# Kernel tuning notes

Hardware: AMD Instinct MI355X
Metric: run time of the kernel (lower is better)

## Reference

```python
import jax, jax.numpy as jnp
import numpy as np
from jax.scipy.linalg import solve_triangular

CHUNK = 32


def _l2norm(x):
    return x / jnp.sqrt(jnp.sum(x * x, axis=-1, keepdims=True))


def setup_inputs() -> dict:
    key = jax.random.key(0)
    kq, kk, kv, kb = jax.random.split(key, 4)
    b, h, L, d = 2, 8, 4096, 128
    q = jax.random.normal(kq, (b, h, L, d), dtype=jnp.float32)
    k = jax.random.normal(kk, (b, h, L, d), dtype=jnp.float32)
    v = jax.random.normal(kv, (b, h, L, d), dtype=jnp.float32)
    beta = jax.random.uniform(kb, (b, h, L), dtype=jnp.float32)
    return {"q": q, "k": k, "v": v, "beta": beta}


def _delta_rule_chunkwise(q, k, v, beta, chunk_size=CHUNK):
    b, h, L, d_k = q.shape
    d_v = v.shape[-1]
    pad_len = (-L) % chunk_size
    if pad_len:
        q = jnp.pad(q, ((0, 0), (0, 0), (0, pad_len), (0, 0)))
        k = jnp.pad(k, ((0, 0), (0, 0), (0, pad_len), (0, 0)))
        v = jnp.pad(v, ((0, 0), (0, 0), (0, pad_len), (0, 0)))
        beta = jnp.pad(beta, ((0, 0), (0, 0), (0, pad_len)))
    L_pad = L + pad_len
    n = L_pad // chunk_size
    c = chunk_size

    q = _l2norm(q)
    k = _l2norm(k)
    v = v * beta[..., None]
    k_beta = k * beta[..., None]

    # -> [b, h, n, c, d]
    qc = q.reshape(b, h, n, c, d_k)
    kc = k.reshape(b, h, n, c, d_k)
    vc = v.reshape(b, h, n, c, d_v)
    kbc = k_beta.reshape(b, h, n, c, d_k)

    # Intra-chunk UT transform: inv = (I + strictly_lower(k_beta @ k^T))^{-1}
    # (equivalent to the sequential forward-substitution loop in the torch code)
    A = jnp.einsum('bhnce,bhnfe->bhncf', kbc, kc)          # [b,h,n,c,c]
    strict_lower = jnp.tril(jnp.ones((c, c), dtype=A.dtype), k=-1)
    T = A * strict_lower + jnp.eye(c, dtype=A.dtype)        # unit lower-triangular
    eye_b = jnp.broadcast_to(jnp.eye(c, dtype=A.dtype), T.shape)
    inv = solve_triangular(T, eye_b, lower=True)            # [b,h,n,c,c]

    u = jnp.einsum('bhncf,bhnfd->bhncd', inv, vc)           # [b,h,n,c,d_v]
    w = jnp.einsum('bhncf,bhnfk->bhnck', inv, kbc)          # [b,h,n,c,d_k]

    # Cross-chunk recurrence over n chunks (sequential in n)
    causal = jnp.tril(jnp.ones((c, c), dtype=q.dtype))      # incl. diagonal
    qs = jnp.moveaxis(qc, 2, 0)   # [n,b,h,c,d_k]
    ks = jnp.moveaxis(kc, 2, 0)
    us = jnp.moveaxis(u, 2, 0)
    ws = jnp.moveaxis(w, 2, 0)

    S0 = jnp.zeros((b, h, d_k, d_v), dtype=q.dtype)

    def step(S, xs):
        q_i, k_i, u_i, w_i = xs
        local_attn = jnp.einsum('bhce,bhfe->bhcf', q_i, k_i) * causal
        u_adj = u_i - jnp.einsum('bhck,bhkd->bhcd', w_i, S)
        o_i = jnp.einsum('bhck,bhkd->bhcd', q_i, S) \
            + jnp.einsum('bhcf,bhfd->bhcd', local_attn, u_adj)
        S_new = S + jnp.einsum('bhck,bhcd->bhkd', k_i, u_adj)
        return S_new, o_i

    S_final, outs = jax.lax.scan(step, S0, (qs, ks, us, ws))
    out = jnp.moveaxis(outs, 0, 2).reshape(b, h, L_pad, d_v)
    if pad_len:
        out = out[:, :, :L]
    return out, S_final


def reference(q, k, v, beta):
    return _delta_rule_chunkwise(q, k, v, beta)
```

## Files before the change

### kernel.cpp

```cpp
#include <hip/hip_runtime.h>


#define Bb 2
#define Hh 8
#define Ll 4096
#define Dd 128
#define DP (Dd + 4)
#define Cc 32
#define CP2 33
#define NC (Ll / Cc)
#define BHn (Bb * Hh)

#define SLAB 20480

typedef float  f32x16 __attribute__((ext_vector_type(16)));
typedef short  bf16x8 __attribute__((ext_vector_type(8)));

__device__ __forceinline__ short f2bf(float x) {
    union { float f; unsigned u; } a; a.f = x;
    const unsigned r = a.u + 0x7FFFu + ((a.u >> 16) & 1u);
    return (short)(r >> 16);
}

__device__ __forceinline__ float bf2f(short h) {
    union { unsigned u; float f; } t;
    t.u = ((unsigned)(unsigned short)h) << 16;
    return t.f;
}

__device__ __forceinline__ unsigned cvt_pk_bf16(float lo, float hi) {
    unsigned r;
    asm("v_cvt_pk_bf16_f32 %0, %1, %2" : "=v"(r) : "v"(lo), "v"(hi));
    return r;
}

__device__ __forceinline__ bf16x8 mk_bop(const f32x16& T, int m) {
    const int o = 8 * m;
    const unsigned a01 = cvt_pk_bf16(T[o + 0], T[o + 1]);
    const unsigned a23 = cvt_pk_bf16(T[o + 2], T[o + 3]);
    const unsigned b01 = cvt_pk_bf16(T[o + 4], T[o + 5]);
    const unsigned b23 = cvt_pk_bf16(T[o + 6], T[o + 7]);
    const auto r0 = __builtin_amdgcn_permlane32_swap(a01, b01, false, false);
    const auto r1 = __builtin_amdgcn_permlane32_swap(a23, b23, false, false);
    union { unsigned u[4]; bf16x8 v; } out;
    out.u[0] = r0[0]; out.u[1] = r1[0]; out.u[2] = r0[1]; out.u[3] = r1[1];
    return out.v;
}

__device__ __forceinline__ void gl_lds16(const void* gsrc, void* ldst) {
    __builtin_amdgcn_global_load_lds(
        (const __attribute__((address_space(1))) unsigned int*)gsrc,
        (__attribute__((address_space(3))) unsigned int*)ldst, 16, 0, 0);
}

__device__ __forceinline__ void split8(const float4& a, const float4& b,
                                       bf16x8& hi, bf16x8& lo) {
    const float x[8] = {a.x, a.y, a.z, a.w, b.x, b.y, b.z, b.w};
    #pragma unroll
    for (int j = 0; j < 8; ++j) {
        const short hs = f2bf(x[j]);
        hi[j] = hs;
        lo[j] = f2bf(x[j] - bf2f(hs));
    }
}

__device__ __forceinline__ void fma4(float4& acc, float s, const float4& x) {
    acc.x += s * x.x; acc.y += s * x.y; acc.z += s * x.z; acc.w += s * x.w;
}

template <bool QNB>
__global__ __launch_bounds__(256, 4) void prep_kernel(
    const float* __restrict__ q, const float* __restrict__ k,
    const float* __restrict__ v, const float* __restrict__ beta,
    float* __restrict__ wsU, float* __restrict__ wsNq,
    short* __restrict__ wsWb, short* __restrict__ wsKtb,
    short* __restrict__ wsAttnb, short* __restrict__ wsQnb)
{
    __shared__ float sK[Cc][DP];
    __shared__ float sA[Cc][CP2];
    __shared__ float sInv[Cc][CP2];
    __shared__ float sBeta[Cc], sNk[Cc], sNq[Cc];

    const int tid = threadIdx.x;
    const int blk = blockIdx.x;
    const int bh = blk / NC;
    const int ch = blk % NC;
    const size_t base = (size_t)(bh * Ll + ch * Cc) * Dd;

    for (int e = tid; e < Cc * Dd / 4; e += 256) {
        const int r = e >> 5, c4 = e & 31;
        ((float4*)&sK[r][0])[c4] = ((const float4*)(k + base))[e];
    }
    if (tid < Cc) sBeta[tid] = beta[bh * Ll + ch * Cc + tid];
    __syncthreads();

    {
        const int row = tid >> 2, part = tid & 3;
        float s = 0.f;
        if (row < Cc) {
            const float4* src = (const float4*)&sK[row][0];
            #pragma unroll
            for (int j = 0; j < 8; ++j) {
                const float4 t = src[part + j * 4];
                s += t.x * t.x + t.y * t.y + t.z * t.z + t.w * t.w;
            }
        } else {
            const float4* src =
                (const float4*)(q + base + (size_t)(row - Cc) * Dd);
            #pragma unroll
            for (int j = 0; j < 8; ++j) {
                const float4 t = src[part + j * 4];
                s += t.x * t.x + t.y * t.y + t.z * t.z + t.w * t.w;
            }
        }
        s += __shfl_xor(s, 1);
        s += __shfl_xor(s, 2);
        if (part == 0) {
            const float r = 1.0f / sqrtf(s);
            if (row < Cc) sNk[row] = r; else sNq[row - Cc] = r;
        }
    }
    __syncthreads();

    if (tid < Cc) wsNq[bh * Ll + ch * Cc + tid] = sNq[tid];

    for (int e = tid; e < Cc * Dd / 4; e += 256) {
        const int r = e >> 5, c4 = e & 31;
        float4 kk = ((float4*)&sK[r][0])[c4];
        const float nk = sNk[r];
        kk.x *= nk; kk.y *= nk; kk.z *= nk; kk.w *= nk;
        ((float4*)&sK[r][0])[c4] = kk;
    }
    __syncthreads();

    const int wid = tid >> 6;
    const int lc = tid & 31;
    const int lh = (tid >> 5) & 1;
    const size_t cbase = (size_t)blk * Cc * Dd;
    const size_t abase = (size_t)blk * Cc * Cc;

    if (wid == 0) {
        f32x16 D, D2;
        #pragma unroll
        for (int r = 0; r < 16; ++r) { D[r] = 0.f; D2[r] = 0.f; }
        #pragma unroll
        for (int ks = 0; ks < 8; ++ks) {
            const float4 a = ((const float4*)&sK[lc][0])[4 * ks + 2 * lh];
            const float4 b = ((const float4*)&sK[lc][0])[4 * ks + 2 * lh + 1];
            bf16x8 hi, lo;
            split8(a, b, hi, lo);
            D  = __builtin_amdgcn_mfma_f32_32x32x16_bf16(hi, hi, D,  0, 0, 0);
            D2 = __builtin_amdgcn_mfma_f32_32x32x16_bf16(hi, lo, D2, 0, 0, 0);
            D2 = __builtin_amdgcn_mfma_f32_32x32x16_bf16(lo, hi, D2, 0, 0, 0);
        }
        #pragma unroll
        for (int r = 0; r < 16; ++r) {
            const int row = (r & 3) + 8 * (r >> 2) + 4 * lh;
            sA[row][lc] = (D[r] + D2[r]) * sBeta[row];
        }
        asm volatile("s_waitcnt lgkmcnt(0)" ::: "memory");
        __builtin_amdgcn_sched_barrier(0);

        float inv[Cc];
        #pragma unroll
        for (int m = 0; m < Cc; ++m) inv[m] = (m == lc) ? 1.f : 0.f;
        #pragma unroll
        for (int i = 1; i < Cc; ++i) {
            float s = 0.f;
            #pragma unroll
            for (int m = 0; m < i; ++m) s += sA[i][m] * inv[m];
            inv[i] = (lc == i) ? 1.f : -s;
        }
        if (lh == 0) {
            #pragma unroll
            for (int m = 0; m < Cc; ++m) sInv[m][lc] = inv[m];
        }
    } else if (wid == 1) {
        const float nq = sNq[lc];
        const float* qrow = q + base + (size_t)lc * Dd;
        f32x16 D, D2;
        #pragma unroll
        for (int r = 0; r < 16; ++r) { D[r] = 0.f; D2[r] = 0.f; }
        #pragma unroll
        for (int ks = 0; ks < 8; ++ks) {
            float4 a = ((const float4*)qrow)[4 * ks + 2 * lh];
            float4 b = ((const float4*)qrow)[4 * ks + 2 * lh + 1];
            a.x *= nq; a.y *= nq; a.z *= nq; a.w *= nq;
            b.x *= nq; b.y *= nq; b.z *= nq; b.w *= nq;
            bf16x8 hiQ, loQ;
            split8(a, b, hiQ, loQ);
            const float4 ka = ((const float4*)&sK[lc][0])[4 * ks + 2 * lh];
            const float4 kb2 = ((const float4*)&sK[lc][0])[4 * ks + 2 * lh + 1];
            bf16x8 hiK, loK;
            split8(ka, kb2, hiK, loK);
            D  = __builtin_amdgcn_mfma_f32_32x32x16_bf16(hiQ, hiK, D,  0, 0, 0);
            D2 = __builtin_amdgcn_mfma_f32_32x32x16_bf16(hiQ, loK, D2, 0, 0, 0);
            D2 = __builtin_amdgcn_mfma_f32_32x32x16_bf16(loQ, hiK, D2, 0, 0, 0);
        }
        #pragma unroll
        for (int r = 0; r < 16; ++r) {
            const int row = (r & 3) + 8 * (r >> 2) + 4 * lh;
            const float val = (lc <= row) ? (D[r] + D2[r]) : 0.f;
            wsAttnb[abase + ((lc >> 3) << 8) + (row << 3) + (lc & 7)] =
                f2bf(val);
        }
    } else {
        const int t = tid - 128;
        #pragma unroll
        for (int it = 0; it < 4; ++it) {
            const int g = t + it * 128;
            const int B = g >> 5, ddl = g & 31;
            const int dd = ((B >> 2) << 5) + ddl;
            const int cc0 = (B & 3) << 3;
            bf16x8 pk;
            #pragma unroll
            for (int j = 0; j < 8; ++j) pk[j] = f2bf(sK[cc0 + j][dd]);
            ((bf16x8*)(wsKtb + cbase))[g] = pk;
        }
        if constexpr (QNB) {
            #pragma unroll
            for (int it = 0; it < 4; ++it) {
                const int g = t + it * 128;
                const int c = g & 31;
                const int dd0 = (g >> 5) << 3;
                const float nq = sNq[c];
                const float4 a =
                    ((const float4*)(q + base + (size_t)c * Dd + dd0))[0];
                const float4 b =
                    ((const float4*)(q + base + (size_t)c * Dd + dd0))[1];
                bf16x8 pk;
                pk[0] = f2bf(a.x * nq); pk[1] = f2bf(a.y * nq);
                pk[2] = f2bf(a.z * nq); pk[3] = f2bf(a.w * nq);
                pk[4] = f2bf(b.x * nq); pk[5] = f2bf(b.y * nq);
                pk[6] = f2bf(b.z * nq); pk[7] = f2bf(b.w * nq);
                ((bf16x8*)(wsQnb + cbase))[g] = pk;
            }
        }
    }
    __syncthreads();

    {
        const int c = tid >> 3, g = tid & 7, dd0 = g * 16;
        float4 u0{}, u1{}, u2{}, u3{}, w0{}, w1{}, w2{}, w3{};
        for (int f = 0; f <= c; ++f) {
            const float ivb = sInv[c][f] * sBeta[f];
            const float4* vr = (const float4*)(v + base + (size_t)f * Dd + dd0);
            const float4* kr = (const float4*)&sK[f][dd0];
            fma4(u0, ivb, vr[0]); fma4(u1, ivb, vr[1]);
            fma4(u2, ivb, vr[2]); fma4(u3, ivb, vr[3]);
            fma4(w0, ivb, kr[0]); fma4(w1, ivb, kr[1]);
            fma4(w2, ivb, kr[2]); fma4(w3, ivb, kr[3]);
        }
        const int rh = (c & 3) + ((c >> 3) << 2) + (((c >> 2) & 1) << 4);
        const float uu[16] = {u0.x, u0.y, u0.z, u0.w, u1.x, u1.y, u1.z, u1.w,
                              u2.x, u2.y, u2.z, u2.w, u3.x, u3.y, u3.z, u3.w};
        #pragma unroll
        for (int j = 0; j < 16; ++j) {
            const int dd = dd0 + j;
            wsU[cbase + ((dd >> 5) << 10) + (rh << 5) + (dd & 31)] = uu[j];
        }
        bf16x8 p0, p1;
        p0[0] = f2bf(-w0.x); p0[1] = f2bf(-w0.y); p0[2] = f2bf(-w0.z);
        p0[3] = f2bf(-w0.w); p0[4] = f2bf(-w1.x); p0[5] = f2bf(-w1.y);
        p0[6] = f2bf(-w1.z); p0[7] = f2bf(-w1.w);
        p1[0] = f2bf(-w2.x); p1[1] = f2bf(-w2.y); p1[2] = f2bf(-w2.z);
        p1[3] = f2bf(-w2.w); p1[4] = f2bf(-w3.x); p1[5] = f2bf(-w3.y);
        p1[6] = f2bf(-w3.z); p1[7] = f2bf(-w3.w);
        ((bf16x8*)(wsWb + cbase))[(2 * g) * 32 + c] = p0;
        ((bf16x8*)(wsWb + cbase))[(2 * g + 1) * 32 + c] = p1;
    }
}

struct RegOps { bf16x8 qa[8]; bf16x8 at[2]; };

template <bool QNB>
__device__ __forceinline__ void load_regs(
    RegOps& R, int bh, int ch, int c, int h,
    const short* __restrict__ wsQnb, const short* __restrict__ wsAttnb)
{
    const size_t cb = (size_t)(bh * NC + ch) * (Cc * Dd);
    const size_t ab = (size_t)(bh * NC + ch) * (Cc * Cc);
    if constexpr (QNB) {
        #pragma unroll
        for (int ks = 0; ks < 8; ++ks)
            R.qa[ks] = ((const bf16x8*)(wsQnb + cb))[(2 * ks + h) * 32 + c];
    }
    R.at[0] = ((const bf16x8*)(wsAttnb + ab))[(0 + h) * 32 + c];
    R.at[1] = ((const bf16x8*)(wsAttnb + ab))[(2 + h) * 32 + c];
}

__device__ __forceinline__ void stage_slab(
    char* slab, int bh, int ch, int colBase, int lane,
    const short* __restrict__ wsWb, const short* __restrict__ wsKtb,
    const float* __restrict__ wsU)
{
    const size_t cb = (size_t)(bh * NC + ch) * (Cc * Dd);
    const char* srcW = (const char*)(wsWb + cb);
    const char* srcK = (const char*)(wsKtb + cb);
    const int l16 = lane * 16;
    #pragma unroll
    for (int g = 0; g < 8; ++g)
        gl_lds16(srcW + g * 1024 + l16, slab + g * 1024);
    #pragma unroll
    for (int g = 0; g < 8; ++g)
        gl_lds16(srcK + g * 1024 + l16, slab + 8192 + g * 1024);
    const float* srcU = wsU + cb + (colBase << 5);
    #pragma unroll
    for (int g = 0; g < 4; ++g)
        gl_lds16(srcU + g * 256 + lane * 4, slab + 16384 + g * 1024);
}

template <bool QNB>
__device__ __forceinline__ void step(
    int ch, char* slab, char* slab2, bool dostage,
    const RegOps& cur, RegOps& nxt,
    int bh, int colBase, int c, int h, int lane,
    const float* __restrict__ q, const float* __restrict__ wsNq,
    const short* __restrict__ wsWb, const short* __restrict__ wsKtb,
    const short* __restrict__ wsAttnb, const short* __restrict__ wsQnb,
    const float* __restrict__ wsU,
    f32x16& S0, f32x16& S1, f32x16& S2, f32x16& S3, float* __restrict__ out)
{
    const int chn = (ch + 1 < NC) ? ch + 1 : NC - 1;
    load_regs<QNB>(nxt, bh, chn, c, h, wsQnb, wsAttnb);

    const bf16x8* Wf = (const bf16x8*)slab;
    const bf16x8* Kf = (const bf16x8*)(slab + 8192);
    const float*  Uf = (const float*)(slab + 16384);

    bf16x8 qa[8];
    if constexpr (QNB) {
        #pragma unroll
        for (int ks = 0; ks < 8; ++ks) qa[ks] = cur.qa[ks];
    } else {
        const size_t qb = (size_t)(bh * Ll + ch * Cc) * Dd;
        const float rq = wsNq[bh * Ll + ch * Cc + c];
        #pragma unroll
        for (int ks = 0; ks < 8; ++ks) {
            const float4 a = ((const float4*)(q + qb))[c * 32 + 4 * ks + 2 * h];
            const float4 b = ((const float4*)(q + qb))[c * 32 + 4 * ks + 2 * h + 1];
            union { unsigned u[4]; bf16x8 v; } t;
            t.u[0] = cvt_pk_bf16(a.x * rq, a.y * rq);
            t.u[1] = cvt_pk_bf16(a.z * rq, a.w * rq);
            t.u[2] = cvt_pk_bf16(b.x * rq, b.y * rq);
            t.u[3] = cvt_pk_bf16(b.z * rq, b.w * rq);
            qa[ks] = t.v;
        }
    }

    f32x16 Ua, Ub, O1, O2;
    #pragma unroll
    for (int r = 0; r < 16; ++r) {
        Ua[r] = Uf[(r + 16 * h) * 32 + c];
        Ub[r] = 0.f; O1[r] = 0.f; O2[r] = 0.f;
    }

    #pragma unroll
    for (int ks = 0; ks < 8; ++ks) {
        const f32x16& T = (ks < 2) ? S0 : (ks < 4) ? S1 : (ks < 6) ? S2 : S3;
        const bf16x8 sB = mk_bop(T, ks & 1);
        const bf16x8 wA = Wf[(2 * ks + h) * 32 + c];
        if (ks < 4)
            Ua = __builtin_amdgcn_mfma_f32_32x32x16_bf16(wA, sB, Ua, 0, 0, 0);
        else
            Ub = __builtin_amdgcn_mfma_f32_32x32x16_bf16(wA, sB, Ub, 0, 0, 0);
        if (ks & 1)
            O2 = __builtin_amdgcn_mfma_f32_32x32x16_bf16(qa[ks], sB, O2, 0, 0, 0);
        else
            O1 = __builtin_amdgcn_mfma_f32_32x32x16_bf16(qa[ks], sB, O1, 0, 0, 0);
    }

    f32x16 Us;
    #pragma unroll
    for (int r = 0; r < 16; ++r) Us[r] = Ua[r] + Ub[r];

    const bf16x8 uB0 = mk_bop(Us, 0);
    const bf16x8 uB1 = mk_bop(Us, 1);

    S0 = __builtin_amdgcn_mfma_f32_32x32x16_bf16(Kf[(0 + h) * 32 + c],  uB0, S0, 0, 0, 0);
    S0 = __builtin_amdgcn_mfma_f32_32x32x16_bf16(Kf[(2 + h) * 32 + c],  uB1, S0, 0, 0, 0);
    S1 = __builtin_amdgcn_mfma_f32_32x32x16_bf16(Kf[(4 + h) * 32 + c],  uB0, S1, 0, 0, 0);
    S1 = __builtin_amdgcn_mfma_f32_32x32x16_bf16(Kf[(6 + h) * 32 + c],  uB1, S1, 0, 0, 0);
    S2 = __builtin_amdgcn_mfma_f32_32x32x16_bf16(Kf[(8 + h) * 32 + c],  uB0, S2, 0, 0, 0);
    S2 = __builtin_amdgcn_mfma_f32_32x32x16_bf16(Kf[(10 + h) * 32 + c], uB1, S2, 0, 0, 0);
    S3 = __builtin_amdgcn_mfma_f32_32x32x16_bf16(Kf[(12 + h) * 32 + c], uB0, S3, 0, 0, 0);
    S3 = __builtin_amdgcn_mfma_f32_32x32x16_bf16(Kf[(14 + h) * 32 + c], uB1, S3, 0, 0, 0);

    O1 = __builtin_amdgcn_mfma_f32_32x32x16_bf16(cur.at[0], uB0, O1, 0, 0, 0);
    O2 = __builtin_amdgcn_mfma_f32_32x32x16_bf16(cur.at[1], uB1, O2, 0, 0, 0);

    if (dostage)
        stage_slab(slab2, bh, ch + 2, colBase, lane, wsWb, wsKtb, wsU);

    const size_t qb = (size_t)(bh * Ll + ch * Cc) * Dd;
    #pragma unroll
    for (int r = 0; r < 16; ++r) {
        const int row = (r & 3) + 8 * (r >> 2) + 4 * h;
        out[qb + (size_t)row * Dd + colBase + c] = O1[r] + O2[r];
    }
}

template <bool QNB>
__global__ __launch_bounds__(64, 1) void scan_kernel(
    const float* __restrict__ q, const float* __restrict__ wsU,
    const short* __restrict__ wsWb, const short* __restrict__ wsKtb,
    const short* __restrict__ wsAttnb, const short* __restrict__ wsQnb,
    const float* __restrict__ wsNq, float* __restrict__ out)
{
    __shared__ __attribute__((aligned(16))) char sl0[SLAB];
    __shared__ __attribute__((aligned(16))) char sl1[SLAB];
    __shared__ __attribute__((aligned(16))) char sl2[SLAB];

    const int lane = threadIdx.x;
    const int h = lane >> 5;
    const int c = lane & 31;
    const int bh = blockIdx.x;
    const int colBase = blockIdx.y * 32;

    f32x16 S0, S1, S2, S3;
    #pragma unroll
    for (int r = 0; r < 16; ++r) { S0[r]=0.f; S1[r]=0.f; S2[r]=0.f; S3[r]=0.f; }

    RegOps R0, R1;
    stage_slab(sl0, bh, 0, colBase, lane, wsWb, wsKtb, wsU);
    stage_slab(sl1, bh, 1, colBase, lane, wsWb, wsKtb, wsU);
    load_regs<QNB>(R0, bh, 0, c, h, wsQnb, wsAttnb);

    #pragma unroll 1
    for (int it = 0; it < 21; ++it) {
        const int ch = it * 6;
        step<QNB>(ch + 0, sl0, sl2, true, R0, R1, bh, colBase, c, h, lane,
                  q, wsNq, wsWb, wsKtb, wsAttnb, wsQnb, wsU, S0, S1, S2, S3, out);
        step<QNB>(ch + 1, sl1, sl0, true, R1, R0, bh, colBase, c, h, lane,
                  q, wsNq, wsWb, wsKtb, wsAttnb, wsQnb, wsU, S0, S1, S2, S3, out);
        step<QNB>(ch + 2, sl2, sl1, true, R0, R1, bh, colBase, c, h, lane,
                  q, wsNq, wsWb, wsKtb, wsAttnb, wsQnb, wsU, S0, S1, S2, S3, out);
        step<QNB>(ch + 3, sl0, sl2, true, R1, R0, bh, colBase, c, h, lane,
                  q, wsNq, wsWb, wsKtb, wsAttnb, wsQnb, wsU, S0, S1, S2, S3, out);
        step<QNB>(ch + 4, sl1, sl0, true, R0, R1, bh, colBase, c, h, lane,
                  q, wsNq, wsWb, wsKtb, wsAttnb, wsQnb, wsU, S0, S1, S2, S3, out);
        step<QNB>(ch + 5, sl2, sl1, true, R1, R0, bh, colBase, c, h, lane,
                  q, wsNq, wsWb, wsKtb, wsAttnb, wsQnb, wsU, S0, S1, S2, S3, out);
    }
    step<QNB>(126, sl0, sl2, false, R0, R1, bh, colBase, c, h, lane,
              q, wsNq, wsWb, wsKtb, wsAttnb, wsQnb, wsU, S0, S1, S2, S3, out);
    step<QNB>(127, sl1, sl0, false, R1, R0, bh, colBase, c, h, lane,
              q, wsNq, wsWb, wsKtb, wsAttnb, wsQnb, wsU, S0, S1, S2, S3, out);

    const size_t soff = (size_t)Bb * Hh * Ll * Dd;
    #pragma unroll
    for (int t = 0; t < 4; ++t) {
        const f32x16& T = (t == 0) ? S0 : (t == 1) ? S1 : (t == 2) ? S2 : S3;
        #pragma unroll
        for (int r = 0; r < 16; ++r) {
            const int row = 32 * t + (r & 3) + 8 * (r >> 2) + 4 * h;
            out[soff + (size_t)bh * Dd * Dd + (size_t)row * Dd + colBase + c] =
                T[r];
        }
    }
}

extern "C" void kernel_launch(void* const* d_in, const int* in_sizes, int n_in,
                              void* d_out, int out_size, void* d_ws,
                              size_t ws_size, hipStream_t stream) {
    const float* q    = (const float*)d_in[0];
    const float* k    = (const float*)d_in[1];
    const float* v    = (const float*)d_in[2];
    const float* beta = (const float*)d_in[3];
    float* out = (float*)d_out;

    const size_t nQK = (size_t)BHn * Ll * Dd;
    float* wsU    = (float*)d_ws;
    float* wsNq   = wsU + nQK;
    short* wsWb   = (short*)(wsNq + (size_t)BHn * Ll);
    short* wsKtb  = wsWb + nQK;
    short* wsAttnb = wsKtb + nQK;
    short* wsQnb  = wsAttnb + (size_t)BHn * NC * Cc * Cc;
    const size_t need_qnb = (size_t)((char*)(wsQnb + nQK) - (char*)d_ws);

    if (ws_size >= need_qnb) {
        prep_kernel<true><<<dim3(BHn * NC), 256, 0, stream>>>(
            q, k, v, beta, wsU, wsNq, wsWb, wsKtb, wsAttnb, wsQnb);
        scan_kernel<true><<<dim3(BHn, 4), 64, 0, stream>>>(
            q, wsU, wsWb, wsKtb, wsAttnb, wsQnb, wsNq, out);
    } else {
        prep_kernel<false><<<dim3(BHn * NC), 256, 0, stream>>>(
            q, k, v, beta, wsU, wsNq, wsWb, wsKtb, wsAttnb, wsQnb);
        scan_kernel<false><<<dim3(BHn, 4), 64, 0, stream>>>(
            q, wsU, wsWb, wsKtb, wsAttnb, wsQnb, wsNq, out);
    }
}
```

Baseline: 349.7 us.

## Split scan into producer and consumer waves with barrier-synchronized LDS triple buffering

The scan kernel now runs two waves per block. One wave only stages the next chunk's W, K, Q, attention and U tiles into LDS and waits on its loads, while the other wave only computes and reads every operand from LDS, with a block barrier after each chunk. Q and attention operands move from register prefetch into the LDS slab, which grows to hold them. The aim is to take global-load issue and latency off the compute wave's serial critical path. In exchange every chunk pays a barrier, and the compute wave does more LDS reads.

```diff
diff --git a/kernel.cpp b/kernel.cpp
--- a/kernel.cpp
+++ b/kernel.cpp
@@ -11,10 +11,12 @@
 #define NC (Ll / Cc)
 #define BHn (Bb * Hh)
 
-#define SLAB 20480
+#define SLAB 30720
 
 typedef float  f32x16 __attribute__((ext_vector_type(16)));
 typedef short  bf16x8 __attribute__((ext_vector_type(8)));
+
+#define WAITVM0 asm volatile("s_waitcnt vmcnt(0)" ::: "memory")
 
 __device__ __forceinline__ short f2bf(float x) {
     union { float f; unsigned u; } a; a.f = x;
@@ -271,32 +273,18 @@
     }
 }
 
-struct RegOps { bf16x8 qa[8]; bf16x8 at[2]; };
-
 template <bool QNB>
-__device__ __forceinline__ void load_regs(
-    RegOps& R, int bh, int ch, int c, int h,
-    const short* __restrict__ wsQnb, const short* __restrict__ wsAttnb)
+__device__ __forceinline__ void stage_slab(
+    char* slab, int bh, int ch, int colBase, int lane,
+    const short* __restrict__ wsWb, const short* __restrict__ wsKtb,
+    const short* __restrict__ wsQnb, const short* __restrict__ wsAttnb,
+    const float* __restrict__ wsU)
 {
     const size_t cb = (size_t)(bh * NC + ch) * (Cc * Dd);
     const size_t ab = (size_t)(bh * NC + ch) * (Cc * Cc);
-    if constexpr (QNB) {
-        #pragma unroll
-        for (int ks = 0; ks < 8; ++ks)
-            R.qa[ks] = ((const bf16x8*)(wsQnb + cb))[(2 * ks + h) * 32 + c];
-    }
-    R.at[0] = ((const bf16x8*)(wsAttnb + ab))[(0 + h) * 32 + c];
-    R.at[1] = ((const bf16x8*)(wsAttnb + ab))[(2 + h) * 32 + c];
-}
-
-__device__ __forceinline__ void stage_slab(
-    char* slab, int bh, int ch, int colBase, int lane,
-    const short* __restrict__ wsWb, const short* __restrict__ wsKtb,
-    const float* __restrict__ wsU)
-{
-    const size_t cb = (size_t)(bh * NC + ch) * (Cc * Dd);
     const char* srcW = (const char*)(wsWb + cb);
     const char* srcK = (const char*)(wsKtb + cb);
+    const char* srcA = (const char*)(wsAttnb + ab);
     const int l16 = lane * 16;
     #pragma unroll
     for (int g = 0; g < 8; ++g)
@@ -304,34 +292,37 @@
     #pragma unroll
     for (int g = 0; g < 8; ++g)
         gl_lds16(srcK + g * 1024 + l16, slab + 8192 + g * 1024);
+    if constexpr (QNB) {
+        const char* srcQ = (const char*)(wsQnb + cb);
+        #pragma unroll
+        for (int g = 0; g < 8; ++g)
+            gl_lds16(srcQ + g * 1024 + l16, slab + 16384 + g * 1024);
+    }
+    #pragma unroll
+    for (int g = 0; g < 2; ++g)
+        gl_lds16(srcA + g * 1024 + l16, slab + 24576 + g * 1024);
     const float* srcU = wsU + cb + (colBase << 5);
     #pragma unroll
     for (int g = 0; g < 4; ++g)
-        gl_lds16(srcU + g * 256 + lane * 4, slab + 16384 + g * 1024);
+        gl_lds16(srcU + g * 256 + lane * 4, slab + 26624 + g * 1024);
 }
 
 template <bool QNB>
-__device__ __forceinline__ void step(
-    int ch, char* slab, char* slab2, bool dostage,
-    const RegOps& cur, RegOps& nxt,
-    int bh, int colBase, int c, int h, int lane,
+__device__ __forceinline__ void compute_chunk(
+    const char* slab, int bh, int ch, int colBase, int c, int h,
     const float* __restrict__ q, const float* __restrict__ wsNq,
-    const short* __restrict__ wsWb, const short* __restrict__ wsKtb,
-    const short* __restrict__ wsAttnb, const short* __restrict__ wsQnb,
-    const float* __restrict__ wsU,
     f32x16& S0, f32x16& S1, f32x16& S2, f32x16& S3, float* __restrict__ out)
 {
-    const int chn = (ch + 1 < NC) ? ch + 1 : NC - 1;
-    load_regs<QNB>(nxt, bh, chn, c, h, wsQnb, wsAttnb);
-
     const bf16x8* Wf = (const bf16x8*)slab;
     const bf16x8* Kf = (const bf16x8*)(slab + 8192);
-    const float*  Uf = (const float*)(slab + 16384);
+    const bf16x8* Qf = (const bf16x8*)(slab + 16384);
+    const bf16x8* Af = (const bf16x8*)(slab + 24576);
+    const float*  Uf = (const float*)(slab + 26624);
 
     bf16x8 qa[8];
     if constexpr (QNB) {
         #pragma unroll
-        for (int ks = 0; ks < 8; ++ks) qa[ks] = cur.qa[ks];
+        for (int ks = 0; ks < 8; ++ks) qa[ks] = Qf[(2 * ks + h) * 32 + c];
     } else {
         const size_t qb = (size_t)(bh * Ll + ch * Cc) * Dd;
         const float rq = wsNq[bh * Ll + ch * Cc + c];
@@ -386,11 +377,8 @@
     S3 = __builtin_amdgcn_mfma_f32_32x32x16_bf16(Kf[(12 + h) * 32 + c], uB0, S3, 0, 0, 0);
     S3 = __builtin_amdgcn_mfma_f32_32x32x16_bf16(Kf[(14 + h) * 32 + c], uB1, S3, 0, 0, 0);
 
-    O1 = __builtin_amdgcn_mfma_f32_32x32x16_bf16(cur.at[0], uB0, O1, 0, 0, 0);
-    O2 = __builtin_amdgcn_mfma_f32_32x32x16_bf16(cur.at[1], uB1, O2, 0, 0, 0);
-
-    if (dostage)
-        stage_slab(slab2, bh, ch + 2, colBase, lane, wsWb, wsKtb, wsU);
+    O1 = __builtin_amdgcn_mfma_f32_32x32x16_bf16(Af[(0 + h) * 32 + c], uB0, O1, 0, 0, 0);
+    O2 = __builtin_amdgcn_mfma_f32_32x32x16_bf16(Af[(2 + h) * 32 + c], uB1, O2, 0, 0, 0);
 
     const size_t qb = (size_t)(bh * Ll + ch * Cc) * Dd;
     #pragma unroll
@@ -401,7 +389,29 @@
 }
 
 template <bool QNB>
-__global__ __launch_bounds__(64, 1) void scan_kernel(
+__device__ __forceinline__ void pcstep(
+    int ch, char* cur, char* nxt, bool dostage, int wid,
+    int bh, int colBase, int c, int h, int lane,
+    const float* __restrict__ q, const float* __restrict__ wsNq,
+    const short* __restrict__ wsWb, const short* __restrict__ wsKtb,
+    const short* __restrict__ wsAttnb, const short* __restrict__ wsQnb,
+    const float* __restrict__ wsU,
+    f32x16& S0, f32x16& S1, f32x16& S2, f32x16& S3, float* __restrict__ out)
+{
+    if (wid == 0) {
+        compute_chunk<QNB>(cur, bh, ch, colBase, c, h, q, wsNq,
+                           S0, S1, S2, S3, out);
+    } else {
+        if (dostage)
+            stage_slab<QNB>(nxt, bh, ch + 2, colBase, lane,
+                            wsWb, wsKtb, wsQnb, wsAttnb, wsU);
+        WAITVM0;
+    }
+    __builtin_amdgcn_s_barrier();
+}
+
+template <bool QNB>
+__global__ __launch_bounds__(128, 1) void scan_kernel(
     const float* __restrict__ q, const float* __restrict__ wsU,
     const short* __restrict__ wsWb, const short* __restrict__ wsKtb,
     const short* __restrict__ wsAttnb, const short* __restrict__ wsQnb,
@@ -411,7 +421,9 @@
     __shared__ __attribute__((aligned(16))) char sl1[SLAB];
     __shared__ __attribute__((aligned(16))) char sl2[SLAB];
 
-    const int lane = threadIdx.x;
+    const int tid = threadIdx.x;
+    const int wid = tid >> 6;
+    const int lane = tid & 63;
     const int h = lane >> 5;
     const int c = lane & 31;
     const int bh = blockIdx.x;
@@ -421,41 +433,44 @@
     #pragma unroll
     for (int r = 0; r < 16; ++r) { S0[r]=0.f; S1[r]=0.f; S2[r]=0.f; S3[r]=0.f; }
 
-    RegOps R0, R1;
-    stage_slab(sl0, bh, 0, colBase, lane, wsWb, wsKtb, wsU);
-    stage_slab(sl1, bh, 1, colBase, lane, wsWb, wsKtb, wsU);
-    load_regs<QNB>(R0, bh, 0, c, h, wsQnb, wsAttnb);
+    if (wid == 1) {
+        stage_slab<QNB>(sl0, bh, 0, colBase, lane, wsWb, wsKtb, wsQnb,
+                        wsAttnb, wsU);
+        stage_slab<QNB>(sl1, bh, 1, colBase, lane, wsWb, wsKtb, wsQnb,
+                        wsAttnb, wsU);
+        WAITVM0;
+    }
+    __builtin_amdgcn_s_barrier();
 
     #pragma unroll 1
-    for (int it = 0; it < 21; ++it) {
-        const int ch = it * 6;
-        step<QNB>(ch + 0, sl0, sl2, true, R0, R1, bh, colBase, c, h, lane,
-                  q, wsNq, wsWb, wsKtb, wsAttnb, wsQnb, wsU, S0, S1, S2, S3, out);
-        step<QNB>(ch + 1, sl1, sl0, true, R1, R0, bh, colBase, c, h, lane,
-                  q, wsNq, wsWb, wsKtb, wsAttnb, wsQnb, wsU, S0, S1, S2, S3, out);
-        step<QNB>(ch + 2, sl2, sl1, true, R0, R1, bh, colBase, c, h, lane,
-                  q, wsNq, wsWb, wsKtb, wsAttnb, wsQnb, wsU, S0, S1, S2, S3, out);
-        step<QNB>(ch + 3, sl0, sl2, true, R1, R0, bh, colBase, c, h, lane,
-                  q, wsNq, wsWb, wsKtb, wsAttnb, wsQnb, wsU, S0, S1, S2, S3, out);
-        step<QNB>(ch + 4, sl1, sl0, true, R0, R1, bh, colBase, c, h, lane,
-                  q, wsNq, wsWb, wsKtb, wsAttnb, wsQnb, wsU, S0, S1, S2, S3, out);
-        step<QNB>(ch + 5, sl2, sl1, true, R1, R0, bh, colBase, c, h, lane,
-                  q, wsNq, wsWb, wsKtb, wsAttnb, wsQnb, wsU, S0, S1, S2, S3, out);
-    }
-    step<QNB>(126, sl0, sl2, false, R0, R1, bh, colBase, c, h, lane,
-              q, wsNq, wsWb, wsKtb, wsAttnb, wsQnb, wsU, S0, S1, S2, S3, out);
-    step<QNB>(127, sl1, sl0, false, R1, R0, bh, colBase, c, h, lane,
-              q, wsNq, wsWb, wsKtb, wsAttnb, wsQnb, wsU, S0, S1, S2, S3, out);
-
-    const size_t soff = (size_t)Bb * Hh * Ll * Dd;
-    #pragma unroll
-    for (int t = 0; t < 4; ++t) {
-        const f32x16& T = (t == 0) ? S0 : (t == 1) ? S1 : (t == 2) ? S2 : S3;
-        #pragma unroll
-        for (int r = 0; r < 16; ++r) {
-            const int row = 32 * t + (r & 3) + 8 * (r >> 2) + 4 * h;
-            out[soff + (size_t)bh * Dd * Dd + (size_t)row * Dd + colBase + c] =
-                T[r];
+    for (int it = 0; it < 42; ++it) {
+        const int ch = it * 3;
+        pcstep<QNB>(ch + 0, sl0, sl2, true, wid, bh, colBase, c, h, lane,
+                    q, wsNq, wsWb, wsKtb, wsAttnb, wsQnb, wsU,
+                    S0, S1, S2, S3, out);
+        pcstep<QNB>(ch + 1, sl1, sl0, true, wid, bh, colBase, c, h, lane,
+                    q, wsNq, wsWb, wsKtb, wsAttnb, wsQnb, wsU,
+                    S0, S1, S2, S3, out);
+        pcstep<QNB>(ch + 2, sl2, sl1, true, wid, bh, colBase, c, h, lane,
+                    q, wsNq, wsWb, wsKtb, wsAttnb, wsQnb, wsU,
+                    S0, S1, S2, S3, out);
+    }
+    pcstep<QNB>(126, sl0, sl2, false, wid, bh, colBase, c, h, lane,
+                q, wsNq, wsWb, wsKtb, wsAttnb, wsQnb, wsU, S0, S1, S2, S3, out);
+    pcstep<QNB>(127, sl1, sl0, false, wid, bh, colBase, c, h, lane,
+                q, wsNq, wsWb, wsKtb, wsAttnb, wsQnb, wsU, S0, S1, S2, S3, out);
+
+    if (wid == 0) {
+        const size_t soff = (size_t)Bb * Hh * Ll * Dd;
+        #pragma unroll
+        for (int t = 0; t < 4; ++t) {
+            const f32x16& T = (t == 0) ? S0 : (t == 1) ? S1 : (t == 2) ? S2 : S3;
+            #pragma unroll
+            for (int r = 0; r < 16; ++r) {
+                const int row = 32 * t + (r & 3) + 8 * (r >> 2) + 4 * h;
+                out[soff + (size_t)bh * Dd * Dd + (size_t)row * Dd + colBase + c]
+                    = T[r];
+            }
         }
     }
 }
@@ -481,12 +496,12 @@
     if (ws_size >= need_qnb) {
         prep_kernel<true><<<dim3(BHn * NC), 256, 0, stream>>>(
             q, k, v, beta, wsU, wsNq, wsWb, wsKtb, wsAttnb, wsQnb);
-        scan_kernel<true><<<dim3(BHn, 4), 64, 0, stream>>>(
+        scan_kernel<true><<<dim3(BHn, 4), 128, 0, stream>>>(
             q, wsU, wsWb, wsKtb, wsAttnb, wsQnb, wsNq, out);
     } else {
         prep_kernel<false><<<dim3(BHn * NC), 256, 0, stream>>>(
             q, k, v, beta, wsU, wsNq, wsWb, wsKtb, wsAttnb, wsQnb);
-        scan_kernel<false><<<dim3(BHn, 4), 64, 0, stream>>>(
+        scan_kernel<false><<<dim3(BHn, 4), 128, 0, stream>>>(
             q, wsU, wsWb, wsKtb, wsAttnb, wsQnb, wsNq, out);
     }
 }
```

New measurement: 316.7 us. 9.4% less time.
